# Kernel optimization log

Hardware: AMD Instinct MI355X
Metric: run time of the kernel (lower is better)

The kernel has to match this reference:

```python
import jax, jax.numpy as jnp
import numpy as np

D_MODEL = 1024
NUM_HEADS = 16
D_K = D_MODEL // NUM_HEADS
B, S = 4, 2048


def setup_inputs() -> dict:
    key = jax.random.key(0)
    ks = jax.random.split(key, 12)
    Q = jax.random.normal(ks[0], (B, S, D_MODEL), dtype=jnp.float32)
    K = jax.random.normal(ks[1], (B, S, D_MODEL), dtype=jnp.float32)
    V = jax.random.normal(ks[2], (B, S, D_MODEL), dtype=jnp.float32)
    # causal mask: 1 where attention allowed, 0 where blocked
    mask = jnp.tril(jnp.ones((S, S), dtype=jnp.int32))[None, None, :, :]
    sc = 1.0 / np.sqrt(D_MODEL)
    Wq = jax.random.normal(ks[3], (D_MODEL, D_MODEL), dtype=jnp.float32) * sc
    Wk = jax.random.normal(ks[4], (D_MODEL, D_MODEL), dtype=jnp.float32) * sc
    Wv = jax.random.normal(ks[5], (D_MODEL, D_MODEL), dtype=jnp.float32) * sc
    Wo = jax.random.normal(ks[6], (D_MODEL, D_MODEL), dtype=jnp.float32) * sc
    bq = jnp.zeros((D_MODEL,), dtype=jnp.float32)
    bk = jnp.zeros((D_MODEL,), dtype=jnp.float32)
    bv = jnp.zeros((D_MODEL,), dtype=jnp.float32)
    bo = jnp.zeros((D_MODEL,), dtype=jnp.float32)
    return {"Q": Q, "K": K, "V": V, "mask": mask,
            "Wq": Wq, "bq": bq, "Wk": Wk, "bk": bk,
            "Wv": Wv, "bv": bv, "Wo": Wo, "bo": bo}


def reference(Q, K, V, mask, Wq, bq, Wk, bk, Wv, bv, Wo, bo):
    b = Q.shape[0]
    # projections (torch Linear: x @ W.T + b; here W stored as [in, out])
    q = Q @ Wq + bq
    k = K @ Wk + bk
    v = V @ Wv + bv
    # [B, S, D] -> [B, H, S, d_k]
    def split_heads(x):
        return x.reshape(b, -1, NUM_HEADS, D_K).transpose(0, 2, 1, 3)
    q, k, v = split_heads(q), split_heads(k), split_heads(v)
    scores = jnp.einsum('bhqd,bhkd->bhqk', q, k) / jnp.sqrt(jnp.float32(D_K))
    scores = jnp.where(mask == 0, -jnp.inf, scores)
    attn = jax.nn.softmax(scores, axis=-1)
    out = jnp.einsum('bhqk,bhkd->bhqd', attn, v)  # [B, H, S, d_k]
    out = out.transpose(0, 2, 1, 3).reshape(b, -1, NUM_HEADS * D_K)
    return out @ Wo + bo
```

## Files before the change

kernel.cpp:

```cpp
#include <hip/hip_runtime.h>

typedef __bf16 bf16_t;
typedef __bf16 bf16x8 __attribute__((ext_vector_type(8)));
typedef __bf16 bf16x4 __attribute__((ext_vector_type(4)));
typedef float  floatx4 __attribute__((ext_vector_type(4)));

#define D_MODEL 1024
#define S_LEN   2048
#define NHEAD   16
#define DK      64
#define BATCH   4
#define MROWS   (BATCH * S_LEN)
#define QSCALE  0.18033688011112042f

__device__ __forceinline__ void load_lds16(const void* gsrc, void* ldst) {
  __builtin_amdgcn_global_load_lds(
      (const __attribute__((address_space(1))) void*)gsrc,
      (__attribute__((address_space(3))) void*)ldst, 16, 0, 0);
}

__device__ __forceinline__ unsigned pack_bf16(float a, float b) {
  union { bf16_t h[2]; unsigned u; } t;
  t.h[0] = (bf16_t)a; t.h[1] = (bf16_t)b;
  return t.u;
}

__device__ __forceinline__ float bperm_f(int addr, float v) {
  union { float f; int i; } in, out;
  in.f = v;
  out.i = __builtin_amdgcn_ds_bpermute(addr, in.i);
  return out.f;
}

__global__ __launch_bounds__(256)
void transpose_w_kernel(const float* __restrict__ W0, const float* __restrict__ W1,
                        const float* __restrict__ W2, const float* __restrict__ W3,
                        bf16_t* __restrict__ T0, bf16_t* __restrict__ T1,
                        bf16_t* __restrict__ T2, bf16_t* __restrict__ T3)
{
  const int z = blockIdx.z;
  const float* W = z == 0 ? W0 : (z == 1 ? W1 : (z == 2 ? W2 : W3));
  bf16_t* Wt     = z == 0 ? T0 : (z == 1 ? T1 : (z == 2 ? T2 : T3));

  __shared__ float tile[64][65];
  const int x0 = blockIdx.x * 64;
  const int y0 = blockIdx.y * 64;
  const int tid = threadIdx.x;
  const int r = tid >> 4;
  const int c = (tid & 15) << 2;
#pragma unroll
  for (int p = 0; p < 4; p++) {
    floatx4 v = *(const floatx4*)&W[(size_t)(y0 + p * 16 + r) * D_MODEL + x0 + c];
    tile[p * 16 + r][c + 0] = v[0];
    tile[p * 16 + r][c + 1] = v[1];
    tile[p * 16 + r][c + 2] = v[2];
    tile[p * 16 + r][c + 3] = v[3];
  }
  __syncthreads();
#pragma unroll
  for (int p = 0; p < 4; p++) {
    int row = p * 16 + r;
    bf16x4 o;
    o[0] = (bf16_t)tile[c + 0][row];
    o[1] = (bf16_t)tile[c + 1][row];
    o[2] = (bf16_t)tile[c + 2][row];
    o[3] = (bf16_t)tile[c + 3][row];
    *(bf16x4*)&Wt[(size_t)(x0 + row) * D_MODEL + y0 + c] = o;
  }
}

__global__ __launch_bounds__(256, 3)
void qkv_kernel(const float* __restrict__ Qi, const float* __restrict__ Ki,
                const float* __restrict__ Vi, const bf16_t* __restrict__ Wcat,
                const float* __restrict__ bq, const float* __restrict__ bk,
                const float* __restrict__ bv,
                bf16_t* __restrict__ qo, bf16_t* __restrict__ ko,
                bf16_t* __restrict__ vo)
{
  __shared__ float  Asf[128 * 32];
  __shared__ bf16_t Bs[128 * 32];

  const int L = blockIdx.x + 24 * blockIdx.y;
  const int j = (L >> 3) & 7;
  const int s = ((L >> 6) << 3) | (L & 7);
  const int z = s >> 6;
  const int n0g = (((z << 3) | j)) << 7;
  const int m0 = (s & 63) << 7;

  const float* A = z == 0 ? Qi : (z == 1 ? Ki : Vi);

  const int tid = threadIdx.x;
  const int lane = tid & 63;
  const int w = tid >> 6;
  const int l15 = lane & 15;
  const int quad = lane >> 4;
  const int wy = (w >> 1) << 6;
  const int wx = (w & 1) << 6;
  const int w64 = w << 6;

  floatx4 acc[4][4];
#pragma unroll
  for (int i = 0; i < 4; i++)
#pragma unroll
    for (int jj = 0; jj < 4; jj++)
#pragma unroll
      for (int r = 0; r < 4; r++) acc[i][jj][r] = 0.0f;

  for (int kt = 0; kt < 32; kt++) {
    const int k0 = kt << 5;
    __syncthreads();
#pragma unroll
    for (int p = 0; p < 2; p++) {
      int slot = p * 256 + w64 + lane;
      int row = slot >> 2;
      int kc = (slot & 3) ^ (row & 3);
      load_lds16(&Wcat[(size_t)(n0g + row) * D_MODEL + k0 + (kc << 3)],
                 &Bs[(size_t)(p * 256 + w64) << 3]);
    }
#pragma unroll
    for (int p = 0; p < 4; p++) {
      int sbase = (w << 8) + (p << 6);
      int slot = sbase + lane;
      int row = slot >> 3;
      int ca = (slot & 7) ^ (row & 7);
      load_lds16(&A[(size_t)(m0 + row) * D_MODEL + k0 + (ca << 2)],
                 &Asf[(size_t)sbase << 2]);
    }
    __syncthreads();

    bf16x8 af[4], bfv[4];
#pragma unroll
    for (int mi = 0; mi < 4; mi++) {
      const int m = wy + mi * 16 + l15;
      const int e = m & 7;
      floatx4 f0 = *(const floatx4*)&Asf[(m << 5) + ((((quad << 1))     ^ e) << 2)];
      floatx4 f1 = *(const floatx4*)&Asf[(m << 5) + ((((quad << 1) | 1) ^ e) << 2)];
      bf16x8 o;
      o[0] = (bf16_t)f0[0]; o[1] = (bf16_t)f0[1];
      o[2] = (bf16_t)f0[2]; o[3] = (bf16_t)f0[3];
      o[4] = (bf16_t)f1[0]; o[5] = (bf16_t)f1[1];
      o[6] = (bf16_t)f1[2]; o[7] = (bf16_t)f1[3];
      af[mi] = o;
    }
#pragma unroll
    for (int ni = 0; ni < 4; ni++) {
      int n = wx + ni * 16 + l15;
      bfv[ni] = *(const bf16x8*)&Bs[n * 32 + ((quad ^ (n & 3)) << 3)];
    }
#pragma unroll
    for (int mi = 0; mi < 4; mi++)
#pragma unroll
      for (int ni = 0; ni < 4; ni++)
        acc[mi][ni] = __builtin_amdgcn_mfma_f32_16x16x32_bf16(
            af[mi], bfv[ni], acc[mi][ni], 0, 0, 0);
  }

  const float* bias = z == 0 ? bq : (z == 1 ? bk : bv);
  bf16_t* outp      = z == 0 ? qo : (z == 1 ? ko : vo);
  const float scl   = (z == 0) ? QSCALE : 1.0f;
#pragma unroll
  for (int mi = 0; mi < 4; mi++) {
#pragma unroll
    for (int ni = 0; ni < 4; ni++) {
      const int nn = (n0g + wx + ni * 16 + l15) & (D_MODEL - 1);
      const float bvv = bias[nn];
      const int h = nn >> 6, d = nn & 63;
#pragma unroll
      for (int r = 0; r < 4; r++) {
        const int m = m0 + wy + mi * 16 + quad * 4 + r;
        const int b = m >> 11, srow = m & (S_LEN - 1);
        float v = (acc[mi][ni][r] + bvv) * scl;
        if (z < 2) {
          outp[((((size_t)(b * NHEAD + h) << 11) + srow) << 6) + d] = (bf16_t)v;
        } else {
          outp[((((size_t)(b * NHEAD + h) << 6) + d) << 11) + srow] = (bf16_t)v;
        }
      }
    }
  }
}

__global__ __launch_bounds__(256)
void out_gemm_kernel(const bf16_t* __restrict__ A, const bf16_t* __restrict__ Wt,
                     const float* __restrict__ bias, float* __restrict__ out)
{
  __shared__ bf16_t As[128 * 32];
  __shared__ bf16_t Bs[128 * 32];
  const int L = blockIdx.x + 8 * blockIdx.y;
  const int n0 = (((L >> 3) & 7)) << 7;
  const int m0 = ((((L >> 6) << 3) | (L & 7))) << 7;
  const int tid = threadIdx.x;
  const int lane = tid & 63;
  const int w = tid >> 6;
  const int l15 = lane & 15;
  const int quad = lane >> 4;
  const int wy = (w >> 1) << 6;
  const int wx = (w & 1) << 6;
  const int w64 = w << 6;

  floatx4 acc[4][4];
#pragma unroll
  for (int i = 0; i < 4; i++)
#pragma unroll
    for (int jj = 0; jj < 4; jj++)
#pragma unroll
      for (int r = 0; r < 4; r++) acc[i][jj][r] = 0.0f;

  for (int kt = 0; kt < 32; kt++) {
    const int k0 = kt << 5;
    __syncthreads();
#pragma unroll
    for (int p = 0; p < 2; p++) {
      int slot = p * 256 + w64 + lane;
      int row = slot >> 2;
      int kc = (slot & 3) ^ (row & 3);
      load_lds16(&A[(size_t)(m0 + row) * D_MODEL + k0 + (kc << 3)],
                 &As[(size_t)(p * 256 + w64) << 3]);
      load_lds16(&Wt[(size_t)(n0 + row) * D_MODEL + k0 + (kc << 3)],
                 &Bs[(size_t)(p * 256 + w64) << 3]);
    }
    __syncthreads();

    bf16x8 af[4], bfv[4];
#pragma unroll
    for (int mi = 0; mi < 4; mi++) {
      int m = wy + mi * 16 + l15;
      af[mi] = *(const bf16x8*)&As[m * 32 + ((quad ^ (m & 3)) << 3)];
    }
#pragma unroll
    for (int ni = 0; ni < 4; ni++) {
      int n = wx + ni * 16 + l15;
      bfv[ni] = *(const bf16x8*)&Bs[n * 32 + ((quad ^ (n & 3)) << 3)];
    }
#pragma unroll
    for (int mi = 0; mi < 4; mi++)
#pragma unroll
      for (int ni = 0; ni < 4; ni++)
        acc[mi][ni] = __builtin_amdgcn_mfma_f32_16x16x32_bf16(
            af[mi], bfv[ni], acc[mi][ni], 0, 0, 0);
  }

#pragma unroll
  for (int mi = 0; mi < 4; mi++) {
#pragma unroll
    for (int ni = 0; ni < 4; ni++) {
      const int nbase = n0 + wx + ni * 16 + l15;
      const float bv = bias[nbase];
#pragma unroll
      for (int r = 0; r < 4; r++) {
        const int m = m0 + wy + mi * 16 + quad * 4 + r;
        out[((size_t)m << 10) + nbase] = acc[mi][ni][r] + bv;
      }
    }
  }
}

__global__ __launch_bounds__(256, 4)
void attn_kernel(const bf16_t* __restrict__ qp, const bf16_t* __restrict__ kp,
                 const bf16_t* __restrict__ vtp, bf16_t* __restrict__ ob)
{
  __shared__ bf16_t Kt0[64 * 64];
  __shared__ bf16_t Kt1[64 * 64];
  __shared__ bf16_t Vt0[64 * 64];
  __shared__ bf16_t Vt1[64 * 64];

  const int pair = blockIdx.x;
  const int bh = blockIdx.y;
  const int tid = threadIdx.x;
  const int w = tid >> 6;
  const int lane = tid & 63;
  const int l15 = lane & 15;
  const int quad = lane >> 4;

  const bf16_t* Qh = qp + ((size_t)bh << 17);
  const bf16_t* Kh = kp + ((size_t)bh << 17);
  const bf16_t* Vh = vtp + ((size_t)bh << 17);
  const int b = bh >> 4, h = bh & 15;

  auto stage = [&](int k0s, bf16_t* dK, bf16_t* dV) {
#pragma unroll
    for (int p = 0; p < 2; p++) {
      const int sbase = (w << 7) + (p << 6);
      const int slot = sbase + lane;
      const int row = slot >> 3;
      const int c = (slot & 7) ^ (row & 7);
      load_lds16(&Kh[((size_t)(k0s + row) << 6) + (c << 3)], &dK[sbase << 3]);
      load_lds16(&Vh[((size_t)row << 11) + k0s + (c << 3)], &dV[sbase << 3]);
    }
  };

  int par = 0;

  auto phase = [&](int qt, bool prefetch_next_phase) {
    const int q0 = qt << 6;
    const int qbase = q0 + (w << 4);
    const int nkb = qt + 1;

    bf16x8 qf[2];
#pragma unroll
    for (int ks = 0; ks < 2; ks++)
      qf[ks] = *(const bf16x8*)&Qh[(size_t)(qbase + l15) * DK +
                                   ks * 32 + (quad << 3)];

    floatx4 acc_o[4];
    float m_i = -1e30f, l_i = 0.0f;
#pragma unroll
    for (int nd = 0; nd < 4; nd++)
#pragma unroll
      for (int r = 0; r < 4; r++) acc_o[nd][r] = 0.0f;

    for (int kb = 0; kb < nkb; kb++) {
      const int k0 = kb << 6;
      __syncthreads();

      const bf16_t* cK = par ? Kt1 : Kt0;
      const bf16_t* cV = par ? Vt1 : Vt0;
      bf16_t* nK = par ? Kt0 : Kt1;
      bf16_t* nV = par ? Vt0 : Vt1;

      if (kb + 1 < nkb)             stage((kb + 1) << 6, nK, nV);
      else if (prefetch_next_phase) stage(0, nK, nV);

      bf16x8 bk[2][4];
#pragma unroll
      for (int ks = 0; ks < 2; ks++)
#pragma unroll
        for (int ni = 0; ni < 4; ni++) {
          const int row = ni * 16 + l15;
          const int cp = ((ks << 2) + quad) ^ (row & 7);
          bk[ks][ni] = *(const bf16x8*)&cK[(row << 6) + (cp << 3)];
        }

      floatx4 st[4];
#pragma unroll
      for (int ni = 0; ni < 4; ni++)
#pragma unroll
        for (int r = 0; r < 4; r++) st[ni][r] = 0.0f;
#pragma unroll
      for (int ks = 0; ks < 2; ks++)
#pragma unroll
        for (int ni = 0; ni < 4; ni++)
          st[ni] = __builtin_amdgcn_mfma_f32_16x16x32_bf16(
              bk[ks][ni], qf[ks], st[ni], 0, 0, 0);

      if (k0 + 63 > qbase) {
        const int qrow = qbase + l15;
#pragma unroll
        for (int ni = 0; ni < 4; ni++) {
          const int keyb = k0 + ni * 16 + quad * 4;
#pragma unroll
          for (int r = 0; r < 4; r++)
            if (keyb + r > qrow) st[ni][r] = -1e30f;
        }
      }

      float v = st[0][0];
#pragma unroll
      for (int ni = 0; ni < 4; ni++)
#pragma unroll
        for (int r = 0; r < 4; r++) v = fmaxf(v, st[ni][r]);
      v = fmaxf(v, __shfl_xor(v, 16));
      v = fmaxf(v, __shfl_xor(v, 32));
      const float mn = fmaxf(m_i, v);
      const float alpha = __builtin_amdgcn_exp2f(m_i - mn);
      m_i = mn;

      unsigned pd[4][2];
      float ssum = 0.0f;
#pragma unroll
      for (int c = 0; c < 4; c++)
#pragma unroll
        for (int hh = 0; hh < 2; hh++) {
          float p0 = __builtin_amdgcn_exp2f(st[c][2 * hh]     - m_i);
          float p1 = __builtin_amdgcn_exp2f(st[c][2 * hh + 1] - m_i);
          ssum += p0 + p1;
          pd[c][hh] = pack_bf16(p0, p1);
        }
      ssum += __shfl_xor(ssum, 16);
      ssum += __shfl_xor(ssum, 32);
      l_i = l_i * alpha + ssum;

#pragma unroll
      for (int r = 0; r < 4; r++) {
        float ab = bperm_f((quad * 4 + r) << 2, alpha);
#pragma unroll
        for (int nd = 0; nd < 4; nd++) acc_o[nd][r] *= ab;
      }

      union AV { unsigned u[4]; bf16x8 v; };
      AV av[2];
#pragma unroll
      for (int ks = 0; ks < 2; ks++)
#pragma unroll
        for (int i = 0; i < 4; i++) {
          const int addr = ((((2 * quad + (i >> 1)) & 3) << 4) | l15) << 2;
          int lo = __builtin_amdgcn_ds_bpermute(addr, (int)pd[ks * 2][i & 1]);
          int hi = __builtin_amdgcn_ds_bpermute(addr, (int)pd[ks * 2 + 1][i & 1]);
          av[ks].u[i] = (unsigned)(quad >= 2 ? hi : lo);
        }

#pragma unroll
      for (int ks = 0; ks < 2; ks++) {
        bf16x8 bvv[4];
#pragma unroll
        for (int nd = 0; nd < 4; nd++) {
          const int row = nd * 16 + l15;
          const int cp = ((ks << 2) + quad) ^ (row & 7);
          bvv[nd] = *(const bf16x8*)&cV[(row << 6) + (cp << 3)];
        }
#pragma unroll
        for (int nd = 0; nd < 4; nd++)
          acc_o[nd] = __builtin_amdgcn_mfma_f32_16x16x32_bf16(
              av[ks].v, bvv[nd], acc_o[nd], 0, 0, 0);
      }

      par ^= 1;
    }

    const float inv = 1.0f / l_i;
#pragma unroll
    for (int r = 0; r < 4; r++) {
      const float linv = bperm_f((quad * 4 + r) << 2, inv);
      const int sRow = qbase + quad * 4 + r;
#pragma unroll
      for (int nd = 0; nd < 4; nd++) {
        const int d = nd * 16 + l15;
        ob[(((size_t)(b * S_LEN + sRow)) << 10) + h * 64 + d] =
            (bf16_t)(acc_o[nd][r] * linv);
      }
    }
  };

  stage(0, Kt0, Vt0);
  phase(31 - pair, true);
  phase(pair, false);
}

extern "C" void kernel_launch(void* const* d_in, const int* in_sizes, int n_in,
                              void* d_out, int out_size, void* d_ws, size_t ws_size,
                              hipStream_t stream)
{
  (void)in_sizes; (void)n_in; (void)out_size; (void)ws_size;
  const float* Q  = (const float*)d_in[0];
  const float* K  = (const float*)d_in[1];
  const float* V  = (const float*)d_in[2];
  const float* Wq = (const float*)d_in[4];
  const float* bq = (const float*)d_in[5];
  const float* Wk = (const float*)d_in[6];
  const float* bk = (const float*)d_in[7];
  const float* Wv = (const float*)d_in[8];
  const float* bv = (const float*)d_in[9];
  const float* Wo = (const float*)d_in[10];
  const float* bo = (const float*)d_in[11];
  float* out = (float*)d_out;

  const size_t NELT = (size_t)MROWS * D_MODEL;
  bf16_t* qp   = (bf16_t*)d_ws;
  bf16_t* kp   = qp + NELT;
  bf16_t* vtp  = kp + NELT;
  bf16_t* obuf = vtp + NELT;
  bf16_t* wqt  = obuf + NELT;
  bf16_t* wkt  = wqt + (size_t)D_MODEL * D_MODEL;
  bf16_t* wvt  = wkt + (size_t)D_MODEL * D_MODEL;
  bf16_t* wot  = wvt + (size_t)D_MODEL * D_MODEL;

  dim3 blk(256);
  transpose_w_kernel<<<dim3(16, 16, 4), blk, 0, stream>>>(
      Wq, Wk, Wv, Wo, wqt, wkt, wvt, wot);

  qkv_kernel<<<dim3(3 * D_MODEL / 128, MROWS / 128), blk, 0, stream>>>(
      Q, K, V, wqt, bq, bk, bv, qp, kp, vtp);

  attn_kernel<<<dim3(16, BATCH * NHEAD), blk, 0, stream>>>(qp, kp, vtp, obuf);

  out_gemm_kernel<<<dim3(D_MODEL / 128, MROWS / 128), blk, 0, stream>>>(
      obuf, wot, bo, out);
}
```

Baseline: 371.9 us.

## Double-buffer LDS tiles in QKV and output projection GEMMs

Both projection GEMM kernels now keep two LDS buffers for the A and B tiles. The async global-to-LDS loads for the next k-tile are issued right after the barrier, so they run while the MFMA work on the current tile proceeds. The goal is to hide global load latency behind compute and to drop one barrier per iteration. In exchange, LDS use per block doubles, and the output GEMM gains a launch bound of 4 blocks per CU, which may constrain register allocation or occupancy.

```diff
diff --git a/kernel.cpp b/kernel.cpp
--- a/kernel.cpp
+++ b/kernel.cpp
@@ -77,8 +77,8 @@
                 bf16_t* __restrict__ qo, bf16_t* __restrict__ ko,
                 bf16_t* __restrict__ vo)
 {
-  __shared__ float  Asf[128 * 32];
-  __shared__ bf16_t Bs[128 * 32];
+  __shared__ float  Asf[2][128 * 32];
+  __shared__ bf16_t Bs[2][128 * 32];
 
   const int L = blockIdx.x + 24 * blockIdx.y;
   const int j = (L >> 3) & 7;
@@ -106,16 +106,15 @@
 #pragma unroll
       for (int r = 0; r < 4; r++) acc[i][jj][r] = 0.0f;
 
-  for (int kt = 0; kt < 32; kt++) {
+  auto stage = [&](int buf, int kt) {
     const int k0 = kt << 5;
-    __syncthreads();
 #pragma unroll
     for (int p = 0; p < 2; p++) {
       int slot = p * 256 + w64 + lane;
       int row = slot >> 2;
       int kc = (slot & 3) ^ (row & 3);
       load_lds16(&Wcat[(size_t)(n0g + row) * D_MODEL + k0 + (kc << 3)],
-                 &Bs[(size_t)(p * 256 + w64) << 3]);
+                 &Bs[buf][(size_t)(p * 256 + w64) << 3]);
     }
 #pragma unroll
     for (int p = 0; p < 4; p++) {
@@ -124,17 +123,26 @@
       int row = slot >> 3;
       int ca = (slot & 7) ^ (row & 7);
       load_lds16(&A[(size_t)(m0 + row) * D_MODEL + k0 + (ca << 2)],
-                 &Asf[(size_t)sbase << 2]);
-    }
+                 &Asf[buf][(size_t)sbase << 2]);
+    }
+  };
+
+  stage(0, 0);
+  int cur = 0;
+
+  for (int kt = 0; kt < 32; kt++) {
     __syncthreads();
+    if (kt + 1 < 32) stage(cur ^ 1, kt + 1);
+    const float*  As_c = Asf[cur];
+    const bf16_t* Bs_c = Bs[cur];
 
     bf16x8 af[4], bfv[4];
 #pragma unroll
     for (int mi = 0; mi < 4; mi++) {
       const int m = wy + mi * 16 + l15;
       const int e = m & 7;
-      floatx4 f0 = *(const floatx4*)&Asf[(m << 5) + ((((quad << 1))     ^ e) << 2)];
-      floatx4 f1 = *(const floatx4*)&Asf[(m << 5) + ((((quad << 1) | 1) ^ e) << 2)];
+      floatx4 f0 = *(const floatx4*)&As_c[(m << 5) + ((((quad << 1))     ^ e) << 2)];
+      floatx4 f1 = *(const floatx4*)&As_c[(m << 5) + ((((quad << 1) | 1) ^ e) << 2)];
       bf16x8 o;
       o[0] = (bf16_t)f0[0]; o[1] = (bf16_t)f0[1];
       o[2] = (bf16_t)f0[2]; o[3] = (bf16_t)f0[3];
@@ -145,7 +153,7 @@
 #pragma unroll
     for (int ni = 0; ni < 4; ni++) {
       int n = wx + ni * 16 + l15;
-      bfv[ni] = *(const bf16x8*)&Bs[n * 32 + ((quad ^ (n & 3)) << 3)];
+      bfv[ni] = *(const bf16x8*)&Bs_c[n * 32 + ((quad ^ (n & 3)) << 3)];
     }
 #pragma unroll
     for (int mi = 0; mi < 4; mi++)
@@ -153,6 +161,8 @@
       for (int ni = 0; ni < 4; ni++)
         acc[mi][ni] = __builtin_amdgcn_mfma_f32_16x16x32_bf16(
             af[mi], bfv[ni], acc[mi][ni], 0, 0, 0);
+
+    cur ^= 1;
   }
 
   const float* bias = z == 0 ? bq : (z == 1 ? bk : bv);
@@ -180,12 +190,12 @@
   }
 }
 
-__global__ __launch_bounds__(256)
+__global__ __launch_bounds__(256, 4)
 void out_gemm_kernel(const bf16_t* __restrict__ A, const bf16_t* __restrict__ Wt,
                      const float* __restrict__ bias, float* __restrict__ out)
 {
-  __shared__ bf16_t As[128 * 32];
-  __shared__ bf16_t Bs[128 * 32];
+  __shared__ bf16_t As[2][128 * 32];
+  __shared__ bf16_t Bs[2][128 * 32];
   const int L = blockIdx.x + 8 * blockIdx.y;
   const int n0 = (((L >> 3) & 7)) << 7;
   const int m0 = ((((L >> 6) << 3) | (L & 7))) << 7;
@@ -206,31 +216,39 @@
 #pragma unroll
       for (int r = 0; r < 4; r++) acc[i][jj][r] = 0.0f;
 
-  for (int kt = 0; kt < 32; kt++) {
+  auto stage = [&](int buf, int kt) {
     const int k0 = kt << 5;
-    __syncthreads();
 #pragma unroll
     for (int p = 0; p < 2; p++) {
       int slot = p * 256 + w64 + lane;
       int row = slot >> 2;
       int kc = (slot & 3) ^ (row & 3);
       load_lds16(&A[(size_t)(m0 + row) * D_MODEL + k0 + (kc << 3)],
-                 &As[(size_t)(p * 256 + w64) << 3]);
+                 &As[buf][(size_t)(p * 256 + w64) << 3]);
       load_lds16(&Wt[(size_t)(n0 + row) * D_MODEL + k0 + (kc << 3)],
-                 &Bs[(size_t)(p * 256 + w64) << 3]);
-    }
+                 &Bs[buf][(size_t)(p * 256 + w64) << 3]);
+    }
+  };
+
+  stage(0, 0);
+  int cur = 0;
+
+  for (int kt = 0; kt < 32; kt++) {
     __syncthreads();
+    if (kt + 1 < 32) stage(cur ^ 1, kt + 1);
+    const bf16_t* As_c = As[cur];
+    const bf16_t* Bs_c = Bs[cur];
 
     bf16x8 af[4], bfv[4];
 #pragma unroll
     for (int mi = 0; mi < 4; mi++) {
       int m = wy + mi * 16 + l15;
-      af[mi] = *(const bf16x8*)&As[m * 32 + ((quad ^ (m & 3)) << 3)];
+      af[mi] = *(const bf16x8*)&As_c[m * 32 + ((quad ^ (m & 3)) << 3)];
     }
 #pragma unroll
     for (int ni = 0; ni < 4; ni++) {
       int n = wx + ni * 16 + l15;
-      bfv[ni] = *(const bf16x8*)&Bs[n * 32 + ((quad ^ (n & 3)) << 3)];
+      bfv[ni] = *(const bf16x8*)&Bs_c[n * 32 + ((quad ^ (n & 3)) << 3)];
     }
 #pragma unroll
     for (int mi = 0; mi < 4; mi++)
@@ -238,6 +256,8 @@
       for (int ni = 0; ni < 4; ni++)
         acc[mi][ni] = __builtin_amdgcn_mfma_f32_16x16x32_bf16(
             af[mi], bfv[ni], acc[mi][ni], 0, 0, 0);
+
+    cur ^= 1;
   }
 
 #pragma unroll
```

Result: slower. 396.7 us (+6.7%).

## Pre-convert QKV inputs to bf16 and use a pipelined 256x256 GEMM

Applied to the files above, without the earlier changes.

A new pre-pass converts the fp32 Q/K/V activations to bf16 in the workspace. The QKV projection then runs as a new 512-thread kernel with 256x256 tiles, swizzled LDS, direct global-to-LDS loads and a double-buffered phase schedule. That schedule interleaves half-tile staging with MFMA bursts and raises wave priority during the MFMAs. This is meant to cut the fp32 load and conversion cost inside the GEMM and to raise MFMA utilisation. The trade-offs are an extra full pass over the inputs, more workspace, and a fallback to the old kernel when the workspace is too small.

```diff
diff --git a/kernel.cpp b/kernel.cpp
--- a/kernel.cpp
+++ b/kernel.cpp
@@ -30,6 +30,30 @@
   in.f = v;
   out.i = __builtin_amdgcn_ds_bpermute(addr, in.i);
   return out.f;
+}
+
+__device__ __forceinline__ void barrier_mem() {
+  asm volatile("" ::: "memory");
+  __builtin_amdgcn_s_barrier();
+  asm volatile("" ::: "memory");
+}
+
+__global__ __launch_bounds__(256)
+void convert_a_kernel(const float* __restrict__ Q, const float* __restrict__ K,
+                      const float* __restrict__ V, bf16_t* __restrict__ Abf)
+{
+  const int z = blockIdx.y;
+  const float* src = z == 0 ? Q : (z == 1 ? K : V);
+  bf16_t* dst = Abf + ((size_t)z << 23);
+  const size_t off = ((size_t)blockIdx.x * 256 + threadIdx.x) * 8;
+  floatx4 a = *(const floatx4*)&src[off];
+  floatx4 b = *(const floatx4*)&src[off + 4];
+  bf16x8 o;
+  o[0] = (bf16_t)a[0]; o[1] = (bf16_t)a[1];
+  o[2] = (bf16_t)a[2]; o[3] = (bf16_t)a[3];
+  o[4] = (bf16_t)b[0]; o[5] = (bf16_t)b[1];
+  o[6] = (bf16_t)b[2]; o[7] = (bf16_t)b[3];
+  *(bf16x8*)&dst[off] = o;
 }
 
 __global__ __launch_bounds__(256)
@@ -69,13 +93,140 @@
   }
 }
 
+__global__ __launch_bounds__(512, 2)
+void qkv8_kernel(const bf16_t* __restrict__ Abf, const bf16_t* __restrict__ Wcat,
+                 const float* __restrict__ bq, const float* __restrict__ bk,
+                 const float* __restrict__ bv,
+                 bf16_t* __restrict__ qo, bf16_t* __restrict__ ko,
+                 bf16_t* __restrict__ vo)
+{
+  __shared__ bf16_t lds[2][2][2][128 * 64];
+
+  const int orig = blockIdx.x;
+  const int L = (orig & 7) * 48 + (orig >> 3);
+  const int bm = L / 12, bn = L % 12;
+  const int m0 = bm << 8;
+  const int n0 = bn << 8;
+  const int z  = n0 >> 10;
+  const bf16_t* A = Abf + ((size_t)z << 23);
+
+  const int tid = threadIdx.x;
+  const int wid = tid >> 6, lane = tid & 63;
+  const int l15 = lane & 15, quad = lane >> 4;
+  const int wm = wid >> 2, wn = wid & 3;
+
+  floatx4 acc[8][4] = {};
+  bf16x8 Af[4][2], Bf[2][2];
+
+  auto stage_half = [&](int buf, int mat, int h, int kt) {
+    const bf16_t* src = mat == 0 ? (A + (size_t)(m0 + (h << 7)) * D_MODEL)
+                                 : (Wcat + (size_t)(n0 + (h << 7)) * D_MODEL);
+    const int k0 = (kt & 15) << 6;
+    bf16_t* dst = &lds[buf][mat][h][0];
+#pragma unroll
+    for (int p = 0; p < 2; p++) {
+      const int slot = (p << 9) + tid;
+      const int row = slot >> 3;
+      const int c = (slot & 7) ^ (row & 7);
+      load_lds16(&src[(size_t)row * D_MODEL + k0 + (c << 3)],
+                 &dst[(size_t)((p << 9) + (wid << 6)) << 3]);
+    }
+  };
+
+#define PHASE(BUF, MH, NH, LDA, LDB, SBUF, SMAT, SH, SKT, VMW)                 \
+  {                                                                            \
+    if (LDA) {                                                                 \
+      _Pragma("unroll") for (int mi = 0; mi < 4; mi++) {                       \
+        const int row = (((MH) * 4 + mi) << 4) + l15;                          \
+        _Pragma("unroll") for (int ks = 0; ks < 2; ks++) {                     \
+          const int ck = (ks << 2) + quad;                                     \
+          Af[mi][ks] = *(const bf16x8*)&lds[BUF][0][wm]                        \
+              [(row << 6) + ((ck ^ (row & 7)) << 3)];                          \
+        }                                                                      \
+      }                                                                        \
+    }                                                                          \
+    if (LDB) {                                                                 \
+      _Pragma("unroll") for (int ni = 0; ni < 2; ni++) {                       \
+        const int row = ((wn & 1) << 6) + (((NH) * 2 + ni) << 4) + l15;        \
+        _Pragma("unroll") for (int ks = 0; ks < 2; ks++) {                     \
+          const int ck = (ks << 2) + quad;                                     \
+          Bf[ni][ks] = *(const bf16x8*)&lds[BUF][1][wn >> 1]                   \
+              [(row << 6) + ((ck ^ (row & 7)) << 3)];                          \
+        }                                                                      \
+      }                                                                        \
+    }                                                                          \
+    stage_half(SBUF, SMAT, SH, SKT);                                           \
+    barrier_mem();                                                             \
+    __builtin_amdgcn_s_setprio(1);                                             \
+    _Pragma("unroll") for (int mi = 0; mi < 4; mi++)                           \
+      _Pragma("unroll") for (int ni = 0; ni < 2; ni++)                         \
+        _Pragma("unroll") for (int ks = 0; ks < 2; ks++)                       \
+          acc[(MH) * 4 + mi][(NH) * 2 + ni] =                                  \
+              __builtin_amdgcn_mfma_f32_16x16x32_bf16(                         \
+                  Af[mi][ks], Bf[ni][ks],                                      \
+                  acc[(MH) * 4 + mi][(NH) * 2 + ni], 0, 0, 0);                 \
+    __builtin_amdgcn_s_setprio(0);                                             \
+    if (VMW) asm volatile("s_waitcnt vmcnt(2)" ::: "memory");                  \
+    barrier_mem();                                                             \
+  }
+
+  stage_half(0, 0, 0, 0);
+  stage_half(0, 0, 1, 0);
+  stage_half(0, 1, 0, 0);
+  stage_half(0, 1, 1, 0);
+  stage_half(1, 0, 0, 1);
+  asm volatile("s_waitcnt vmcnt(2)" ::: "memory");
+  barrier_mem();
+
+  for (int it = 0; it < 8; it++) {
+    const int t1 = 2 * it + 1;
+    const int t2 = 2 * it + 2;
+    const int t3 = 2 * it + 3;
+    PHASE(0, 0, 0, 1, 1, 1, 0, 1, t1, 0)
+    PHASE(0, 0, 1, 0, 1, 1, 1, 0, t1, 0)
+    PHASE(0, 1, 1, 1, 0, 1, 1, 1, t1, 0)
+    PHASE(0, 1, 0, 0, 1, 0, 0, 0, t2, 1)
+    PHASE(1, 0, 0, 1, 1, 0, 0, 1, t2, 0)
+    PHASE(1, 0, 1, 0, 1, 0, 1, 0, t2, 0)
+    PHASE(1, 1, 1, 1, 0, 0, 1, 1, t2, 0)
+    PHASE(1, 1, 0, 0, 1, 1, 0, 0, t3, 1)
+  }
+  asm volatile("s_waitcnt vmcnt(0)" ::: "memory");
+
+#undef PHASE
+
+  const float* bias = z == 0 ? bq : (z == 1 ? bk : bv);
+  bf16_t* outp      = z == 0 ? qo : (z == 1 ? ko : vo);
+  const float scl   = (z == 0) ? QSCALE : 1.0f;
+#pragma unroll
+  for (int mi = 0; mi < 8; mi++) {
+#pragma unroll
+    for (int ni = 0; ni < 4; ni++) {
+      const int nn = (n0 + (wn << 6) + (ni << 4) + l15) & (D_MODEL - 1);
+      const float bvv = bias[nn];
+      const int h = nn >> 6, d = nn & 63;
+#pragma unroll
+      for (int r = 0; r < 4; r++) {
+        const int m = m0 + (wm << 7) + (mi << 4) + quad * 4 + r;
+        const int b = m >> 11, srow = m & (S_LEN - 1);
+        float v = (acc[mi][ni][r] + bvv) * scl;
+        if (z < 2) {
+          outp[((((size_t)(b * NHEAD + h) << 11) + srow) << 6) + d] = (bf16_t)v;
+        } else {
+          outp[((((size_t)(b * NHEAD + h) << 6) + d) << 11) + srow] = (bf16_t)v;
+        }
+      }
+    }
+  }
+}
+
 __global__ __launch_bounds__(256, 3)
-void qkv_kernel(const float* __restrict__ Qi, const float* __restrict__ Ki,
-                const float* __restrict__ Vi, const bf16_t* __restrict__ Wcat,
-                const float* __restrict__ bq, const float* __restrict__ bk,
-                const float* __restrict__ bv,
-                bf16_t* __restrict__ qo, bf16_t* __restrict__ ko,
-                bf16_t* __restrict__ vo)
+void qkv_legacy_kernel(const float* __restrict__ Qi, const float* __restrict__ Ki,
+                       const float* __restrict__ Vi, const bf16_t* __restrict__ Wcat,
+                       const float* __restrict__ bq, const float* __restrict__ bk,
+                       const float* __restrict__ bv,
+                       bf16_t* __restrict__ qo, bf16_t* __restrict__ ko,
+                       bf16_t* __restrict__ vo)
 {
   __shared__ float  Asf[128 * 32];
   __shared__ bf16_t Bs[128 * 32];
@@ -440,7 +591,7 @@
                               void* d_out, int out_size, void* d_ws, size_t ws_size,
                               hipStream_t stream)
 {
-  (void)in_sizes; (void)n_in; (void)out_size; (void)ws_size;
+  (void)in_sizes; (void)n_in; (void)out_size;
   const float* Q  = (const float*)d_in[0];
   const float* K  = (const float*)d_in[1];
   const float* V  = (const float*)d_in[2];
@@ -455,21 +606,33 @@
   float* out = (float*)d_out;
 
   const size_t NELT = (size_t)MROWS * D_MODEL;
+  const size_t WELT = (size_t)D_MODEL * D_MODEL;
+
+  const size_t need_new = (3 * NELT + 4 * WELT + 3 * NELT) * sizeof(bf16_t);
+
   bf16_t* qp   = (bf16_t*)d_ws;
   bf16_t* kp   = qp + NELT;
   bf16_t* vtp  = kp + NELT;
-  bf16_t* obuf = vtp + NELT;
-  bf16_t* wqt  = obuf + NELT;
-  bf16_t* wkt  = wqt + (size_t)D_MODEL * D_MODEL;
-  bf16_t* wvt  = wkt + (size_t)D_MODEL * D_MODEL;
-  bf16_t* wot  = wvt + (size_t)D_MODEL * D_MODEL;
+  bf16_t* wqt  = vtp + NELT;
+  bf16_t* wkt  = wqt + WELT;
+  bf16_t* wvt  = wkt + WELT;
+  bf16_t* wot  = wvt + WELT;
+  bf16_t* abf  = wot + WELT;
+  bf16_t* obuf = abf;
 
   dim3 blk(256);
   transpose_w_kernel<<<dim3(16, 16, 4), blk, 0, stream>>>(
       Wq, Wk, Wv, Wo, wqt, wkt, wvt, wot);
 
-  qkv_kernel<<<dim3(3 * D_MODEL / 128, MROWS / 128), blk, 0, stream>>>(
-      Q, K, V, wqt, bq, bk, bv, qp, kp, vtp);
+  if (ws_size >= need_new) {
+    convert_a_kernel<<<dim3(MROWS * D_MODEL / (256 * 8), 3), blk, 0, stream>>>(
+        Q, K, V, abf);
+    qkv8_kernel<<<dim3((MROWS / 256) * (3 * D_MODEL / 256)), dim3(512), 0,
+                  stream>>>(abf, wqt, bq, bk, bv, qp, kp, vtp);
+  } else {
+    qkv_legacy_kernel<<<dim3(3 * D_MODEL / 128, MROWS / 128), blk, 0, stream>>>(
+        Q, K, V, wqt, bq, bk, bv, qp, kp, vtp);
+  }
 
   attn_kernel<<<dim3(16, BATCH * NHEAD), blk, 0, stream>>>(qp, kp, vtp, obuf);
 
```

Result: no change. 366.9 us (-1.3%).
